# Kernel tuning notes

Hardware: AMD Instinct MI355X
Metric: run time of the kernel (lower is better)

Reference implementation:

```python
import jax, jax.numpy as jnp
from jax import lax
import numpy as np

B, H, W = 16, 512, 512
OPENING_R, EROSION_R, DILATION_R = 5, 2, 1
MIN_SIZE, AREA_THRESHOLD = 2000, 300
INF = np.int32(2 ** 30)


def _disk(r):
    # skimage.morphology.disk: x^2 + y^2 <= r^2 on a (2r+1)^2 grid
    y, x = np.mgrid[-r:r + 1, -r:r + 1]
    return jnp.asarray((x * x + y * y <= r * r).astype(np.float32))


D_OPEN, D_ERODE, D_DILATE = _disk(OPENING_R), _disk(EROSION_R), _disk(DILATION_R)


def _conv2(x, k):
    return lax.conv_general_dilated(x[None, None], k[None, None], (1, 1), 'VALID')[0, 0]


def _erode(fg, se):
    # skimage binary_erosion uses border_value=True (image border does not erode)
    r = se.shape[0] // 2
    x = jnp.pad(fg.astype(jnp.float32), r, constant_values=1.0)
    return _conv2(x, se) >= se.sum() - 0.5


def _dilate(fg, se):
    # skimage binary_dilation uses border_value=False
    r = se.shape[0] // 2
    x = jnp.pad(fg.astype(jnp.float32), r, constant_values=0.0)
    return _conv2(x, se) > 0.5


def _seg_cummin(v, reset, axis, reverse):
    # segmented cumulative-min: scan resets wherever `reset` is True (background)
    def comb(a, b):
        av, af = a
        bv, bf = b
        return jnp.where(bf, bv, jnp.minimum(av, bv)), af | bf

    vv, _ = lax.associative_scan(comb, (v, reset), axis=axis, reverse=reverse)
    return vv


def _label(fg):
    # 4-connectivity connected-component labeling via min-label propagation.
    # Each fg pixel starts with its raveled index; alternating row/col segmented
    # cummin sweeps run under while_loop until a fixed point (root id per comp).
    h, w = fg.shape
    idx = jnp.arange(h * w, dtype=jnp.int32).reshape(h, w)
    lab0 = jnp.where(fg, idx, INF)
    bg = ~fg

    def sweep(l):
        for axis in (1, 0):
            for rev in (False, True):
                l = jnp.where(fg, _seg_cummin(l, bg, axis, rev), INF)
        return l

    def body(c):
        l, _ = c
        nl = sweep(l)
        return nl, jnp.array_equal(nl, l)

    lab, _ = lax.while_loop(lambda c: ~c[1], body, (lab0, jnp.array(False)))
    seg = jnp.where(fg, lab, 0).ravel()
    sizes = jax.ops.segment_sum(fg.astype(jnp.int32).ravel(), seg, num_segments=h * w)
    ncomp = jnp.sum(sizes > 0)
    return lab, sizes, ncomp


def _remove_small_objects(fg, min_size, guard):
    lab, sizes, ncomp = _label(fg)
    px = sizes[jnp.where(fg, lab, 0)]  # component size at every fg pixel
    kept = fg & (px >= min_size)
    # original only removes small objects when label(...).max() > 1
    return jnp.where(ncomp > 1, kept, fg) if guard else kept


def _pipeline(mask):
    fg = mask > 0
    fg = _remove_small_objects(fg, MIN_SIZE, True)
    # remove_small_holes == ~remove_small_objects(~fg, area_threshold + 1)
    fg = ~_remove_small_objects(~fg, AREA_THRESHOLD + 1, False)
    fg = _erode(fg, D_ERODE)
    fg = _dilate(_erode(fg, D_OPEN), D_OPEN)  # binary_opening
    fg = _remove_small_objects(fg, MIN_SIZE, True)
    fg = _dilate(fg, D_DILATE)
    return fg.astype(jnp.float32)  # original casts to int; float32 kept for vjp parity


def setup_inputs() -> dict:
    key = jax.random.key(0)
    # blobby binary masks: threshold bilinearly-upsampled low-res noise so that
    # realistic large connected components (> min_size px) exist
    low = jax.random.uniform(key, (B, H // 16, W // 16), dtype=jnp.float32)
    blob = jax.image.resize(low, (B, H, W), method='bilinear')
    return {'inputs': (blob > 0.5).astype(jnp.float32)}


def reference(inputs):
    return jax.vmap(_pipeline)(inputs)
```

## Files before the change

### kernel.cpp

```cpp
#include <hip/hip_runtime.h>
#include <stdint.h>

#define BATCH 16
#define H 512
#define W 512
#define HW (H * W)
#define NTOT (BATCH * HW)
#define NWORDS (NTOT / 64)

#define TPB 256
#define NBLK ((NTOT + TPB - 1) / TPB)
#define NBLKW ((NWORDS + TPB - 1) / TPB)

#define SROWS 16
#define SWORDS 128
#define SPIX 8192
#define NSTRIPS (NWORDS / SWORDS)

__device__ __forceinline__ int find_root_c(int* L, int x) {
    int r = x, p = L[r];
    while (p != r) { r = p; p = L[r]; }
    if (L[x] != r) atomicMin(&L[x], r);
    return r;
}

__device__ void merge_uf(int* L, int a, int b) {
    while (true) {
        a = find_root_c(L, a);
        b = find_root_c(L, b);
        if (a == b) return;
        int lo = a < b ? a : b;
        int hi = a < b ? b : a;
        int old = atomicMin(&L[hi], lo);
        if (old == hi) return;
        a = lo; b = old;
    }
}

__device__ __forceinline__ int find_root_lds(int* P, int x) {
    int r = x, p = P[r];
    while (p != r) { r = p; p = P[r]; }
    return r;
}

__device__ void merge_lds(int* P, int a, int b) {
    while (true) {
        a = find_root_lds(P, a);
        b = find_root_lds(P, b);
        if (a == b) return;
        int lo = a < b ? a : b;
        int hi = a < b ? b : a;
        int old = atomicMin(&P[hi], lo);
        if (old == hi) return;
        a = lo; b = old;
    }
}

__device__ __forceinline__ int start_of(uint64_t m, int i, int cv, int base) {
    uint64_t below = i ? ((~m) & ((1ull << i) - 1)) : 0ull;
    if (below == 0) return (cv >= 0) ? cv : base;
    int hz = 63 - __builtin_clzll(below);
    return base + hz + 1;
}

__device__ uint64_t keep_word(const uint64_t* __restrict__ bits,
                              const int* __restrict__ carry, const int* __restrict__ L,
                              const int* __restrict__ sizes, const int* __restrict__ ncomp,
                              int minsz, int gw) {
    uint64_t m = bits[gw];
    uint64_t res = m;
    if (m && ncomp[gw >> 12] > 1) {
        int cv = carry[gw];
        int base = gw << 6;
        while (m) {
            int s = __builtin_ctzll(m);
            uint64_t rest = m >> s;
            uint64_t nr = ~rest;
            int len = nr ? __builtin_ctzll(nr) : (64 - s);
            uint64_t piece = ((len >= 64) ? ~0ull : ((1ull << len) - 1)) << s;
            int start = (s == 0 && cv >= 0) ? cv : (base + s);
            if (sizes[L[start]] < minsz) res &= ~piece;
            m &= ~piece;
        }
    }
    return res;
}

__device__ uint64_t fill_word(const uint64_t* __restrict__ bits,
                              const int* __restrict__ carry, const int* __restrict__ L,
                              const int* __restrict__ sizes, int minsz, int gw) {
    uint64_t fg = bits[gw];
    uint64_t bg = ~fg;
    uint64_t res = fg;
    int cv = carry[gw];
    int base = gw << 6;
    while (bg) {
        int s = __builtin_ctzll(bg);
        uint64_t rest = bg >> s;
        uint64_t nr = ~rest;
        int len = nr ? __builtin_ctzll(nr) : (64 - s);
        uint64_t piece = ((len >= 64) ? ~0ull : ((1ull << len) - 1)) << s;
        int start = (s == 0 && cv >= 0) ? cv : (base + s);
        if (sizes[L[start]] < minsz) res |= piece;
        bg &= ~piece;
    }
    return res;
}

template <int R, bool ERODE>
__device__ uint64_t morph_word_lds(const uint64_t* buf, int lrow, int w, int gyTop) {
    const uint64_t BORDER = ERODE ? ~0ull : 0ull;
    uint64_t res = ERODE ? ~0ull : 0ull;
#pragma unroll
    for (int dy = -R; dy <= R; ++dy) {
        int lr = lrow + dy;
        int gy = gyTop + lr;
        if (gy < 0 || gy >= H) continue;
        int v = R * R - dy * dy;
        int kx = 0;
        while ((kx + 1) * (kx + 1) <= v) ++kx;
        uint64_t cur = buf[lr * 8 + w];
        uint64_t prv = (w > 0) ? buf[lr * 8 + w - 1] : BORDER;
        uint64_t nxt = (w < 7) ? buf[lr * 8 + w + 1] : BORDER;
        uint64_t acc = cur;
#pragma unroll
        for (int dx = 1; dx <= kx; ++dx) {
            uint64_t right = (cur >> dx) | (nxt << (64 - dx));
            uint64_t left  = (cur << dx) | (prv >> (64 - dx));
            if (ERODE) acc &= right & left;
            else       acc |= right | left;
        }
        if (ERODE) res &= acc;
        else       res |= acc;
    }
    return res;
}

__device__ void strip_ccl_body(uint64_t m, uint64_t* sw, int* scarry, int* par,
                               int blk, int t,
                               int* __restrict__ carry, int* __restrict__ L,
                               int* __restrict__ sizes, int* __restrict__ ncomp) {
    sw[t] = m;
    __syncthreads();

    if (t < SROWS) {
        int cv = -1;
        for (int i = 0; i < 8; ++i) {
            int lw = t * 8 + i;
            scarry[lw] = cv;
            uint64_t w = sw[lw];
            if (w >> 63) {
                uint64_t z = ~w;
                if (z == 0) { if (cv < 0) cv = lw << 6; }
                else { int hz = 63 - __builtin_clzll(z); cv = (lw << 6) + hz + 1; }
            } else cv = -1;
        }
    }
    __syncthreads();

    int cv = scarry[t];
    carry[blk * SWORDS + t] = (cv >= 0) ? (blk * SPIX + cv) : -1;
    int lbase = t << 6;
    uint64_t starts = m & ~((m << 1) | ((cv >= 0) ? 1ull : 0ull));
    uint64_t ss = starts;
    while (ss) {
        int s = __builtin_ctzll(ss);
        par[lbase + s] = lbase + s;
        ss &= ss - 1;
    }
    __syncthreads();

    if (t >= 8 && m) {
        uint64_t up = sw[t - 8];
        uint64_t cand = m & up;
        if (cand) {
            uint64_t curprev = (t & 7) ? sw[t - 1] : 0ull;
            uint64_t upprev  = (t & 7) ? sw[t - 9] : 0ull;
            uint64_t curl = (m << 1) | (curprev >> 63);
            uint64_t upl  = (up << 1) | (upprev >> 63);
            cand &= ~(curl & upl);
            int cvu = scarry[t - 8];
            while (cand) {
                int i = __builtin_ctzll(cand);
                int sP = start_of(m, i, cv, lbase);
                int sQ = start_of(up, i, cvu, lbase - 512);
                merge_lds(par, sP, sQ);
                cand &= cand - 1;
            }
        }
    }
    __syncthreads();

    int gpix = blk * SPIX;
    ss = starts;
    while (ss) {
        int s = __builtin_ctzll(ss);
        int ls = lbase + s;
        int r = find_root_lds(par, ls);
        L[gpix + ls] = gpix + r;
        if (r == ls) sizes[gpix + ls] = 0;
        ss &= ss - 1;
    }
    if (t == 0 && (blk & 31) == 0) ncomp[blk >> 5] = 0;
}


__global__ void k_thresh_ccl(const float* __restrict__ in, uint64_t* __restrict__ bits,
                             int* __restrict__ carry, int* __restrict__ L,
                             int* __restrict__ sizes, int* __restrict__ ncomp) {
    __shared__ uint64_t sw[SWORDS];
    __shared__ int scarry[SWORDS];
    __shared__ int par[SPIX];
    int blk = blockIdx.x;
    int t = threadIdx.x;
    int wave = t >> 6, lane = t & 63;
    size_t stripPix = (size_t)blk * SPIX;
    for (int k = 0; k < 64; ++k) {
        bool a = in[stripPix + wave * 4096 + k * 64 + lane] > 0.0f;
        uint64_t b = __ballot(a);
        if (lane == 0) sw[wave * 64 + k] = b;
    }
    __syncthreads();
    uint64_t m = sw[t];
    bits[blk * SWORDS + t] = m;
    strip_ccl_body(m, sw, scarry, par, blk, t, carry, L, sizes, ncomp);
}

__global__ void k_strip_ccl(const uint64_t* __restrict__ bits, int inv,
                            int* __restrict__ carry, int* __restrict__ L,
                            int* __restrict__ sizes, int* __restrict__ ncomp) {
    __shared__ uint64_t sw[SWORDS];
    __shared__ int scarry[SWORDS];
    __shared__ int par[SPIX];
    int blk = blockIdx.x;
    int t = threadIdx.x;
    uint64_t inv64 = inv ? ~0ull : 0ull;
    uint64_t m = bits[blk * SWORDS + t] ^ inv64;
    strip_ccl_body(m, sw, scarry, par, blk, t, carry, L, sizes, ncomp);
}

__global__ void k_merge_bound(const uint64_t* __restrict__ bits, int inv,
                              const int* __restrict__ carry, int* __restrict__ L) {
    int tid = threadIdx.x;
    if (tid >= 248) return;
    int img = blockIdx.x;
    int y = ((tid >> 3) + 1) * SROWS;
    int w = tid & 7;
    int gw = img * 4096 + y * 8 + w;
    uint64_t inv64 = inv ? ~0ull : 0ull;
    uint64_t cur = bits[gw] ^ inv64;
    uint64_t up  = bits[gw - 8] ^ inv64;
    uint64_t cand = cur & up;
    if (!cand) return;
    uint64_t curprev = w ? (bits[gw - 1] ^ inv64) : 0ull;
    uint64_t upprev  = w ? (bits[gw - 9] ^ inv64) : 0ull;
    uint64_t curl = (cur << 1) | (curprev >> 63);
    uint64_t upl  = (up << 1)  | (upprev >> 63);
    cand &= ~(curl & upl);
    if (!cand) return;
    int cvc = carry[gw], cvu = carry[gw - 8];
    int base = gw << 6;
    while (cand) {
        int i = __builtin_ctzll(cand);
        int sP = start_of(cur, i, cvc, base);
        int sQ = start_of(up, i, cvu, base - W);
        merge_uf(L, sP, sQ);
        cand &= cand - 1;
    }
}

__global__ void k_flatten_count(const uint64_t* __restrict__ bits, int inv,
                                const int* __restrict__ carry, int* __restrict__ L,
                                int* __restrict__ sizes, int* __restrict__ ncomp) {
    __shared__ int hk[128];
    __shared__ int hv[128];
    for (int i = threadIdx.x; i < 128; i += TPB) { hk[i] = -1; hv[i] = 0; }
    __syncthreads();

    int gw = blockIdx.x * blockDim.x + threadIdx.x;
    if (gw < NWORDS) {
        uint64_t inv64 = inv ? ~0ull : 0ull;
        uint64_t m = bits[gw] ^ inv64;
        if (m) {
            int cv = carry[gw];
            int base = gw << 6;
            while (m) {
                int s = __builtin_ctzll(m);
                uint64_t rest = m >> s;
                uint64_t nr = ~rest;
                int len = nr ? __builtin_ctzll(nr) : (64 - s);
                uint64_t piece = ((len >= 64) ? ~0ull : ((1ull << len) - 1)) << s;
                bool initial = !(s == 0 && cv >= 0);
                int start = initial ? (base + s) : cv;
                int r = find_root_c(L, start);
                if (initial && r == start) atomicAdd(&ncomp[gw >> 12], 1);
                int cnt = __popcll(piece);
                uint32_t h = ((uint32_t)r * 2654435761u) >> 25;
                bool done = false;
                for (int tt = 0; tt < 16; ++tt) {
                    int slot = (h + tt) & 127;
                    int k = hk[slot];
                    if (k == -1) k = atomicCAS(&hk[slot], -1, r);
                    if (k == -1 || k == r) { atomicAdd(&hv[slot], cnt); done = true; break; }
                }
                if (!done) atomicAdd(&sizes[r], cnt);
                m &= ~piece;
            }
        }
    }
    __syncthreads();
    for (int i = threadIdx.x; i < 128; i += TPB)
        if (hk[i] != -1) atomicAdd(&sizes[hk[i]], hv[i]);
}

__global__ void k_keep_guard(const uint64_t* __restrict__ bits,
                             const int* __restrict__ carry, const int* __restrict__ L,
                             const int* __restrict__ sizes, const int* __restrict__ ncomp,
                             int minsz, uint64_t* __restrict__ out) {
    int gw = blockIdx.x * blockDim.x + threadIdx.x;
    if (gw >= NWORDS) return;
    out[gw] = keep_word(bits, carry, L, sizes, ncomp, minsz, gw);
}

__global__ void k_fill_morph(const uint64_t* __restrict__ bits,
                             const int* __restrict__ carry, const int* __restrict__ L,
                             const int* __restrict__ sizes,
                             uint64_t* __restrict__ out) {
    __shared__ uint64_t bufA[88 * 8];
    __shared__ uint64_t bufB[88 * 8];
    int img = blockIdx.x >> 3;
    int s   = blockIdx.x & 7;
    int y0 = s * 64;
    int gyTop = y0 - 12;
    int t = threadIdx.x;

    for (int lw = t; lw < 88 * 8; lw += TPB) {
        int gy = gyTop + (lw >> 3);
        int w = lw & 7;
        uint64_t v = 0;
        if (gy >= 0 && gy < H)
            v = fill_word(bits, carry, L, sizes, 301, img * 4096 + gy * 8 + w);
        bufA[lw] = v;
    }
    __syncthreads();

    for (int lw = t; lw < 88 * 8; lw += TPB) {
        int lr = lw >> 3;
        if (lr < 2 || lr > 85) continue;
        bufB[lw] = morph_word_lds<2, true>(bufA, lr, lw & 7, gyTop);
    }
    __syncthreads();

    for (int lw = t; lw < 88 * 8; lw += TPB) {
        int lr = lw >> 3;
        if (lr < 7 || lr > 80) continue;
        bufA[lw] = morph_word_lds<5, true>(bufB, lr, lw & 7, gyTop);
    }
    __syncthreads();

    for (int lw = t; lw < 88 * 8; lw += TPB) {
        int lr = lw >> 3;
        if (lr < 12 || lr > 75) continue;
        uint64_t v = morph_word_lds<5, false>(bufA, lr, lw & 7, gyTop);
        int gy = gyTop + lr;
        out[img * 4096 + gy * 8 + (lw & 7)] = v;
    }
}

__global__ void k_keep_dilate_float(const uint64_t* __restrict__ bits,
                                    const int* __restrict__ carry, const int* __restrict__ L,
                                    const int* __restrict__ sizes, const int* __restrict__ ncomp,
                                    float* __restrict__ out) {
    int p = blockIdx.x * blockDim.x + threadIdx.x;
    if (p >= NTOT) return;
    int gw = p >> 6;
    int lane = threadIdx.x & 63;
    int w = gw & 7;
    int y = (gw >> 3) & (H - 1);
    int target = -1;
    if      (lane == 0) target = gw;
    else if (lane == 1) target = (y > 0)     ? gw - 8 : -1;
    else if (lane == 2) target = (y < H - 1) ? gw + 8 : -1;
    else if (lane == 3) target = (w > 0)     ? gw - 1 : -1;
    else if (lane == 4) target = (w < 7)     ? gw + 1 : -1;
    uint64_t tv = (target >= 0)
        ? keep_word(bits, carry, L, sizes, ncomp, 2000, target) : 0ull;
    uint64_t cur = __shfl(tv, 0);
    uint64_t up  = __shfl(tv, 1);
    uint64_t dn  = __shfl(tv, 2);
    uint64_t prv = __shfl(tv, 3);
    uint64_t nxt = __shfl(tv, 4);
    uint64_t d = cur | up | dn | (cur << 1) | (prv >> 63) | (cur >> 1) | (nxt << 63);
    out[p] = ((d >> lane) & 1ull) ? 1.0f : 0.0f;
}

extern "C" void kernel_launch(void* const* d_in, const int* in_sizes, int n_in,
                              void* d_out, int out_size, void* d_ws, size_t ws_size,
                              hipStream_t stream) {
    const float* in = (const float*)d_in[0];
    float* out = (float*)d_out;

    uint8_t* ws = (uint8_t*)d_ws;
    int* labels = (int*)ws;
    int* sizes  = (int*)(ws + (size_t)NTOT * 4);
    uint64_t* bitsA = (uint64_t*)(ws + (size_t)NTOT * 8);
    uint64_t* bitsB = bitsA + NWORDS;
    int* carry = (int*)(bitsB + NWORDS);
    int* ncomp = carry + NWORDS;

    k_thresh_ccl<<<NSTRIPS, SWORDS, 0, stream>>>(in, bitsA, carry, labels, sizes, ncomp);
    k_merge_bound<<<BATCH, 256, 0, stream>>>(bitsA, 0, carry, labels);
    k_flatten_count<<<NBLKW, TPB, 0, stream>>>(bitsA, 0, carry, labels, sizes, ncomp);
    k_keep_guard<<<NBLKW, TPB, 0, stream>>>(bitsA, carry, labels, sizes, ncomp, 2000, bitsB);

    k_strip_ccl<<<NSTRIPS, SWORDS, 0, stream>>>(bitsB, 1, carry, labels, sizes, ncomp);
    k_merge_bound<<<BATCH, 256, 0, stream>>>(bitsB, 1, carry, labels);
    k_flatten_count<<<NBLKW, TPB, 0, stream>>>(bitsB, 1, carry, labels, sizes, ncomp);

    k_fill_morph<<<BATCH * 8, TPB, 0, stream>>>(bitsB, carry, labels, sizes, bitsA);

    k_strip_ccl<<<NSTRIPS, SWORDS, 0, stream>>>(bitsA, 0, carry, labels, sizes, ncomp);
    k_merge_bound<<<BATCH, 256, 0, stream>>>(bitsA, 0, carry, labels);
    k_flatten_count<<<NBLKW, TPB, 0, stream>>>(bitsA, 0, carry, labels, sizes, ncomp);

    k_keep_dilate_float<<<NBLK, TPB, 0, stream>>>(bitsA, carry, labels, sizes, ncomp, out);
}
```

Baseline: 231.9 us.

## Split threshold packing from strip CCL, halve morph tiles, separate final keep pass

Thresholding and bit packing move out of the first strip-CCL kernel into a standalone fully parallel ballot kernel, and the first CCL reuses the generic strip kernel. The fill+morphology kernel now processes 32-row tiles instead of 64, doubling block count at the cost of proportionally more halo recomputation. The final keep-small-objects filter moves out of the per-pixel float kernel, where 5 lanes per wave redundantly ran the label walk, into a word-level keep_guard pass. A simple dilate-to-float kernel follows it, adding one launch and extra memory traffic.

Measured after the change: 212.6 us. 8.3% less time.

```diff
diff --git a/kernel.cpp b/kernel.cpp
--- a/kernel.cpp
+++ b/kernel.cpp
@@ -61,29 +61,6 @@
     if (below == 0) return (cv >= 0) ? cv : base;
     int hz = 63 - __builtin_clzll(below);
     return base + hz + 1;
-}
-
-__device__ uint64_t keep_word(const uint64_t* __restrict__ bits,
-                              const int* __restrict__ carry, const int* __restrict__ L,
-                              const int* __restrict__ sizes, const int* __restrict__ ncomp,
-                              int minsz, int gw) {
-    uint64_t m = bits[gw];
-    uint64_t res = m;
-    if (m && ncomp[gw >> 12] > 1) {
-        int cv = carry[gw];
-        int base = gw << 6;
-        while (m) {
-            int s = __builtin_ctzll(m);
-            uint64_t rest = m >> s;
-            uint64_t nr = ~rest;
-            int len = nr ? __builtin_ctzll(nr) : (64 - s);
-            uint64_t piece = ((len >= 64) ? ~0ull : ((1ull << len) - 1)) << s;
-            int start = (s == 0 && cv >= 0) ? cv : (base + s);
-            if (sizes[L[start]] < minsz) res &= ~piece;
-            m &= ~piece;
-        }
-    }
-    return res;
 }
 
 __device__ uint64_t fill_word(const uint64_t* __restrict__ bits,
@@ -136,10 +113,23 @@
     return res;
 }
 
-__device__ void strip_ccl_body(uint64_t m, uint64_t* sw, int* scarry, int* par,
-                               int blk, int t,
-                               int* __restrict__ carry, int* __restrict__ L,
-                               int* __restrict__ sizes, int* __restrict__ ncomp) {
+__global__ void k_thresh_pack(const float* __restrict__ in, uint64_t* __restrict__ bits) {
+    int p = blockIdx.x * blockDim.x + threadIdx.x;
+    bool a = (p < NTOT) && (in[p] > 0.0f);
+    uint64_t b = __ballot(a);
+    if ((threadIdx.x & 63) == 0 && p < NTOT) bits[p >> 6] = b;
+}
+
+__global__ void k_strip_ccl(const uint64_t* __restrict__ bits, int inv,
+                            int* __restrict__ carry, int* __restrict__ L,
+                            int* __restrict__ sizes, int* __restrict__ ncomp) {
+    __shared__ uint64_t sw[SWORDS];
+    __shared__ int scarry[SWORDS];
+    __shared__ int par[SPIX];
+    int blk = blockIdx.x;
+    int t = threadIdx.x;
+    uint64_t inv64 = inv ? ~0ull : 0ull;
+    uint64_t m = bits[blk * SWORDS + t] ^ inv64;
     sw[t] = m;
     __syncthreads();
 
@@ -202,41 +192,6 @@
         ss &= ss - 1;
     }
     if (t == 0 && (blk & 31) == 0) ncomp[blk >> 5] = 0;
-}
-
-
-__global__ void k_thresh_ccl(const float* __restrict__ in, uint64_t* __restrict__ bits,
-                             int* __restrict__ carry, int* __restrict__ L,
-                             int* __restrict__ sizes, int* __restrict__ ncomp) {
-    __shared__ uint64_t sw[SWORDS];
-    __shared__ int scarry[SWORDS];
-    __shared__ int par[SPIX];
-    int blk = blockIdx.x;
-    int t = threadIdx.x;
-    int wave = t >> 6, lane = t & 63;
-    size_t stripPix = (size_t)blk * SPIX;
-    for (int k = 0; k < 64; ++k) {
-        bool a = in[stripPix + wave * 4096 + k * 64 + lane] > 0.0f;
-        uint64_t b = __ballot(a);
-        if (lane == 0) sw[wave * 64 + k] = b;
-    }
-    __syncthreads();
-    uint64_t m = sw[t];
-    bits[blk * SWORDS + t] = m;
-    strip_ccl_body(m, sw, scarry, par, blk, t, carry, L, sizes, ncomp);
-}
-
-__global__ void k_strip_ccl(const uint64_t* __restrict__ bits, int inv,
-                            int* __restrict__ carry, int* __restrict__ L,
-                            int* __restrict__ sizes, int* __restrict__ ncomp) {
-    __shared__ uint64_t sw[SWORDS];
-    __shared__ int scarry[SWORDS];
-    __shared__ int par[SPIX];
-    int blk = blockIdx.x;
-    int t = threadIdx.x;
-    uint64_t inv64 = inv ? ~0ull : 0ull;
-    uint64_t m = bits[blk * SWORDS + t] ^ inv64;
-    strip_ccl_body(m, sw, scarry, par, blk, t, carry, L, sizes, ncomp);
 }
 
 __global__ void k_merge_bound(const uint64_t* __restrict__ bits, int inv,
@@ -319,22 +274,38 @@
                              int minsz, uint64_t* __restrict__ out) {
     int gw = blockIdx.x * blockDim.x + threadIdx.x;
     if (gw >= NWORDS) return;
-    out[gw] = keep_word(bits, carry, L, sizes, ncomp, minsz, gw);
+    uint64_t m = bits[gw];
+    uint64_t res = m;
+    if (m && ncomp[gw >> 12] > 1) {
+        int cv = carry[gw];
+        int base = gw << 6;
+        while (m) {
+            int s = __builtin_ctzll(m);
+            uint64_t rest = m >> s;
+            uint64_t nr = ~rest;
+            int len = nr ? __builtin_ctzll(nr) : (64 - s);
+            uint64_t piece = ((len >= 64) ? ~0ull : ((1ull << len) - 1)) << s;
+            int start = (s == 0 && cv >= 0) ? cv : (base + s);
+            if (sizes[L[start]] < minsz) res &= ~piece;
+            m &= ~piece;
+        }
+    }
+    out[gw] = res;
 }
 
 __global__ void k_fill_morph(const uint64_t* __restrict__ bits,
                              const int* __restrict__ carry, const int* __restrict__ L,
                              const int* __restrict__ sizes,
                              uint64_t* __restrict__ out) {
-    __shared__ uint64_t bufA[88 * 8];
-    __shared__ uint64_t bufB[88 * 8];
-    int img = blockIdx.x >> 3;
-    int s   = blockIdx.x & 7;
-    int y0 = s * 64;
+    __shared__ uint64_t bufA[56 * 8];
+    __shared__ uint64_t bufB[56 * 8];
+    int img = blockIdx.x >> 4;
+    int s   = blockIdx.x & 15;
+    int y0 = s * 32;
     int gyTop = y0 - 12;
     int t = threadIdx.x;
 
-    for (int lw = t; lw < 88 * 8; lw += TPB) {
+    for (int lw = t; lw < 56 * 8; lw += TPB) {
         int gy = gyTop + (lw >> 3);
         int w = lw & 7;
         uint64_t v = 0;
@@ -344,54 +315,44 @@
     }
     __syncthreads();
 
-    for (int lw = t; lw < 88 * 8; lw += TPB) {
+    for (int lw = t; lw < 56 * 8; lw += TPB) {
         int lr = lw >> 3;
-        if (lr < 2 || lr > 85) continue;
+        if (lr < 2 || lr > 53) continue;
         bufB[lw] = morph_word_lds<2, true>(bufA, lr, lw & 7, gyTop);
     }
     __syncthreads();
 
-    for (int lw = t; lw < 88 * 8; lw += TPB) {
+    for (int lw = t; lw < 56 * 8; lw += TPB) {
         int lr = lw >> 3;
-        if (lr < 7 || lr > 80) continue;
+        if (lr < 7 || lr > 48) continue;
         bufA[lw] = morph_word_lds<5, true>(bufB, lr, lw & 7, gyTop);
     }
     __syncthreads();
 
-    for (int lw = t; lw < 88 * 8; lw += TPB) {
+    for (int lw = t; lw < 56 * 8; lw += TPB) {
         int lr = lw >> 3;
-        if (lr < 12 || lr > 75) continue;
+        if (lr < 12 || lr > 43) continue;
         uint64_t v = morph_word_lds<5, false>(bufA, lr, lw & 7, gyTop);
         int gy = gyTop + lr;
         out[img * 4096 + gy * 8 + (lw & 7)] = v;
     }
 }
 
-__global__ void k_keep_dilate_float(const uint64_t* __restrict__ bits,
-                                    const int* __restrict__ carry, const int* __restrict__ L,
-                                    const int* __restrict__ sizes, const int* __restrict__ ncomp,
-                                    float* __restrict__ out) {
+__global__ void k_to_float_dilate(const uint64_t* __restrict__ bits,
+                                  float* __restrict__ out) {
     int p = blockIdx.x * blockDim.x + threadIdx.x;
     if (p >= NTOT) return;
     int gw = p >> 6;
-    int lane = threadIdx.x & 63;
+    int i = p & 63;
     int w = gw & 7;
     int y = (gw >> 3) & (H - 1);
-    int target = -1;
-    if      (lane == 0) target = gw;
-    else if (lane == 1) target = (y > 0)     ? gw - 8 : -1;
-    else if (lane == 2) target = (y < H - 1) ? gw + 8 : -1;
-    else if (lane == 3) target = (w > 0)     ? gw - 1 : -1;
-    else if (lane == 4) target = (w < 7)     ? gw + 1 : -1;
-    uint64_t tv = (target >= 0)
-        ? keep_word(bits, carry, L, sizes, ncomp, 2000, target) : 0ull;
-    uint64_t cur = __shfl(tv, 0);
-    uint64_t up  = __shfl(tv, 1);
-    uint64_t dn  = __shfl(tv, 2);
-    uint64_t prv = __shfl(tv, 3);
-    uint64_t nxt = __shfl(tv, 4);
+    uint64_t cur = bits[gw];
+    uint64_t up  = (y > 0)     ? bits[gw - 8] : 0ull;
+    uint64_t dn  = (y < H - 1) ? bits[gw + 8] : 0ull;
+    uint64_t prv = (w > 0)     ? bits[gw - 1] : 0ull;
+    uint64_t nxt = (w < 7)     ? bits[gw + 1] : 0ull;
     uint64_t d = cur | up | dn | (cur << 1) | (prv >> 63) | (cur >> 1) | (nxt << 63);
-    out[p] = ((d >> lane) & 1ull) ? 1.0f : 0.0f;
+    out[p] = ((d >> i) & 1ull) ? 1.0f : 0.0f;
 }
 
 extern "C" void kernel_launch(void* const* d_in, const int* in_sizes, int n_in,
@@ -408,7 +369,9 @@
     int* carry = (int*)(bitsB + NWORDS);
     int* ncomp = carry + NWORDS;
 
-    k_thresh_ccl<<<NSTRIPS, SWORDS, 0, stream>>>(in, bitsA, carry, labels, sizes, ncomp);
+    k_thresh_pack<<<NBLK, TPB, 0, stream>>>(in, bitsA);
+
+    k_strip_ccl<<<NSTRIPS, SWORDS, 0, stream>>>(bitsA, 0, carry, labels, sizes, ncomp);
     k_merge_bound<<<BATCH, 256, 0, stream>>>(bitsA, 0, carry, labels);
     k_flatten_count<<<NBLKW, TPB, 0, stream>>>(bitsA, 0, carry, labels, sizes, ncomp);
     k_keep_guard<<<NBLKW, TPB, 0, stream>>>(bitsA, carry, labels, sizes, ncomp, 2000, bitsB);
@@ -417,11 +380,12 @@
     k_merge_bound<<<BATCH, 256, 0, stream>>>(bitsB, 1, carry, labels);
     k_flatten_count<<<NBLKW, TPB, 0, stream>>>(bitsB, 1, carry, labels, sizes, ncomp);
 
-    k_fill_morph<<<BATCH * 8, TPB, 0, stream>>>(bitsB, carry, labels, sizes, bitsA);
+    k_fill_morph<<<BATCH * 16, TPB, 0, stream>>>(bitsB, carry, labels, sizes, bitsA);
 
     k_strip_ccl<<<NSTRIPS, SWORDS, 0, stream>>>(bitsA, 0, carry, labels, sizes, ncomp);
     k_merge_bound<<<BATCH, 256, 0, stream>>>(bitsA, 0, carry, labels);
     k_flatten_count<<<NBLKW, TPB, 0, stream>>>(bitsA, 0, carry, labels, sizes, ncomp);
-
-    k_keep_dilate_float<<<NBLK, TPB, 0, stream>>>(bitsA, carry, labels, sizes, ncomp, out);
-}
+    k_keep_guard<<<NBLKW, TPB, 0, stream>>>(bitsA, carry, labels, sizes, ncomp, 2000, bitsB);
+
+    k_to_float_dilate<<<NBLK, TPB, 0, stream>>>(bitsB, out);
+}
```
